# Kernel optimization log

Hardware: AMD Instinct MI355X
Metric: run time of the kernel (lower is better)

The kernel has to match this reference:

```python
import jax, jax.numpy as jnp
import numpy as np

G = 8192          # graphs in batch
A = 5             # num_agents (nodes per graph)
N = G * A         # total nodes
IN_CH = 29
HID = 64
HEADS = 8
D = HID * HEADS   # 512, node/graph feature dim
NOPT = 4
ADIM = 3


def _lin(key, fan_in, fan_out):
    return jax.random.normal(key, (fan_in, fan_out), jnp.float32) / np.sqrt(fan_in)


def setup_inputs() -> dict:
    key = jax.random.key(0)
    ks = jax.random.split(key, 40)
    # --- graph structure: G fully-connected 5-node graphs + self loops ---
    pairs = np.array([(i, j) for i in range(A) for j in range(A) if i != j])  # [20,2]
    base = (np.arange(G)[:, None] * A)
    src = (base + pairs[None, :, 0]).reshape(-1)
    dst = (base + pairs[None, :, 1]).reshape(-1)
    # GATConv adds self loops (fill_value=0.0 for edge_attr)
    loop = np.arange(N)
    edge_src = jnp.asarray(np.concatenate([src, loop]), jnp.int32)
    edge_dst = jnp.asarray(np.concatenate([dst, loop]), jnp.int32)
    e_real = jax.random.uniform(ks[0], (src.shape[0], 1), jnp.float32)
    edge_attr = jnp.concatenate([e_real, jnp.zeros((N, 1), jnp.float32)], axis=0)
    batch_map = jnp.asarray(np.repeat(np.arange(G), A), jnp.int32)
    x = jax.random.normal(ks[1], (N, IN_CH), jnp.float32)
    sc = 1.0 / np.sqrt(HID)
    inp = dict(
        x=x, edge_attr=edge_attr, edge_src=edge_src, edge_dst=edge_dst, batch_map=batch_map,
        # conv1
        W1=_lin(ks[2], IN_CH, D), as1=jax.random.normal(ks[3], (HEADS, HID)) * sc,
        ad1=jax.random.normal(ks[4], (HEADS, HID)) * sc, We1=_lin(ks[5], 1, D),
        ae1=jax.random.normal(ks[6], (HEADS, HID)) * sc, b1=jnp.zeros((D,), jnp.float32),
        # conv2
        W2=_lin(ks[7], D, D), as2=jax.random.normal(ks[8], (HEADS, HID)) * sc,
        ad2=jax.random.normal(ks[9], (HEADS, HID)) * sc, We2=_lin(ks[10], 1, D),
        ae2=jax.random.normal(ks[11], (HEADS, HID)) * sc, b2=jnp.zeros((D,), jnp.float32),
        # policy-over-options head
        pw1=_lin(ks[12], D, 2 * HID), pb1=jnp.zeros((2 * HID,)), pw2=_lin(ks[13], 2 * HID, NOPT), pb2=jnp.zeros((NOPT,)),
        # q-options head
        qw1=_lin(ks[14], D, 2 * HID), qb1=jnp.zeros((2 * HID,)), qw2=_lin(ks[15], 2 * HID, NOPT), qb2=jnp.zeros((NOPT,)),
        # intra-option actor head (option 0), input dim = node + graph feature = 2*D
        aw1=_lin(ks[16], 2 * D, 2 * HID), ab1=jnp.zeros((2 * HID,)), aw2=_lin(ks[17], 2 * HID, 2 * ADIM), ab2=jnp.zeros((2 * ADIM,)),
        # termination head (option 0)
        tw1=_lin(ks[18], D, HID), tb1=jnp.zeros((HID,)), tw2=_lin(ks[19], HID, 1), tb2=jnp.zeros((1,)),
        action_limits=jnp.array([1.0, 1.0, 3.14159], jnp.float32),
    )
    return inp


def _gat(x, src, dst, eattr, W, a_s, a_d, We, a_e, b):
    n = x.shape[0]
    h = (x @ W).reshape(n, HEADS, HID)                      # [N,H,C]
    e = (eattr @ We).reshape(-1, HEADS, HID)                # [E,H,C]
    lg = ((h * a_s).sum(-1)[src] + (h * a_d).sum(-1)[dst]
          + (e * a_e).sum(-1))                              # [E,H]
    lg = jnp.where(lg > 0, lg, 0.2 * lg)                    # leaky_relu(0.2)
    m = jax.ops.segment_max(lg, dst, num_segments=n)
    p = jnp.exp(lg - m[dst])
    denom = jax.ops.segment_sum(p, dst, num_segments=n)[dst] + 1e-16
    alpha = p / denom                                       # scatter-softmax over dst
    out = jax.ops.segment_sum(alpha[:, :, None] * h[src], dst, num_segments=n)
    return out.reshape(n, HEADS * HID) + b


def reference(x, edge_attr, edge_src, edge_dst, batch_map,
              W1, as1, ad1, We1, ae1, b1,
              W2, as2, ad2, We2, ae2, b2,
              pw1, pb1, pw2, pb2, qw1, qb1, qw2, qb2,
              aw1, ab1, aw2, ab2, tw1, tb1, tw2, tb2, action_limits):
    h = jax.nn.relu(_gat(x, edge_src, edge_dst, edge_attr, W1, as1, ad1, We1, ae1, b1))
    h = jax.nn.relu(_gat(h, edge_src, edge_dst, edge_attr, W2, as2, ad2, We2, ae2, b2))
    # global_mean_pool
    cnt = jax.ops.segment_sum(jnp.ones((h.shape[0],), h.dtype), batch_map, num_segments=G)
    g = jax.ops.segment_sum(h, batch_map, num_segments=G) / cnt[:, None]   # [G,D]
    pi = jax.nn.relu(g @ pw1 + pb1) @ pw2 + pb2                            # [G,NOPT]
    q = jax.nn.relu(g @ qw1 + qb1) @ qw2 + qb2                             # [G,NOPT]
    term = jax.nn.sigmoid(jax.nn.relu(g @ tw1 + tb1) @ tw2 + tb2)          # [G,1]
    # per-graph first num_agents nodes == all nodes here (5 per graph)
    agent = h.reshape(G, A, D)
    comb = jnp.concatenate([agent, jnp.broadcast_to(g[:, None, :], (G, A, D))], axis=-1)
    ho = jax.nn.relu(comb @ aw1 + ab1) @ aw2 + ab2                          # [G,A,6]
    mean_raw, log_std_raw = jnp.split(ho, 2, axis=-1)
    mean = jnp.tanh(mean_raw) * action_limits                               # [G,A,3]
    std = 0.05 + jax.nn.sigmoid(log_std_raw) * 0.45 + 1e-6
    return jnp.concatenate([pi, q, term, mean.reshape(G, -1), std.reshape(G, -1)], axis=1)
```

## Files before the change

kernel.cpp:

```cpp
#include <hip/hip_runtime.h>
#include <hip/hip_bf16.h>
#include <math.h>

#define GG 8192
#define AA 5
#define NN (GG * AA)
#define DD 512

typedef unsigned short ushort_t;
typedef unsigned int uint_t;

__device__ inline float bf2f(ushort_t u) {
  union { uint_t i; float f; } c; c.i = ((uint_t)u) << 16; return c.f;
}
__device__ inline ushort_t f2bf(float f) {
  union { float f; uint_t i; } c; c.f = f;
  uint_t r = c.i + 0x7fffu + ((c.i >> 16) & 1u);
  return (ushort_t)(r >> 16);
}

using frag8 = __attribute__((ext_vector_type(8))) short;
using f32x4 = __attribute__((ext_vector_type(4))) float;

typedef __attribute__((address_space(3))) void lds_void;
typedef __attribute__((address_space(1))) const void gbl_void;
#define GLL(g, l) __builtin_amdgcn_global_load_lds((gbl_void*)(g), (lds_void*)(l), 16, 0, 0)

__device__ inline int xcd_swz(int bid, int nwg) {
  return (bid & 7) * (nwg >> 3) + (bid >> 3);
}

__global__ __launch_bounds__(256) void k_prep(
    const float* __restrict__ x, const float* __restrict__ W1,
    const float* __restrict__ W2, const float* __restrict__ pw1,
    const float* __restrict__ qw1, const float* __restrict__ tw1,
    const float* __restrict__ aw1, const float* __restrict__ pb1,
    const float* __restrict__ qb1, const float* __restrict__ tb1,
    const float* __restrict__ ab1, const float* __restrict__ We1,
    const float* __restrict__ ae1, const float* __restrict__ We2,
    const float* __restrict__ ae2, const float* __restrict__ as1,
    const float* __restrict__ ad1, const float* __restrict__ as2,
    const float* __restrict__ ad2, const float* __restrict__ pw2,
    const float* __restrict__ pb2, const float* __restrict__ qw2,
    const float* __restrict__ qb2, const float* __restrict__ tw2,
    const float* __restrict__ tb2, const float* __restrict__ aw2,
    const float* __restrict__ ab2, ushort_t* __restrict__ xpad32,
    ushort_t* __restrict__ W1T32, ushort_t* __restrict__ W2T,
    ushort_t* __restrict__ WcatT, ushort_t* __restrict__ aw1topT,
    ushort_t* __restrict__ wsc1T, ushort_t* __restrict__ wsc2T,
    float* __restrict__ bcat, float* __restrict__ sce,
    float* __restrict__ woutT, float* __restrict__ bout) {
  int b = blockIdx.x;
  int t = threadIdx.x;
  if (b < 1024) {
    int i = b * 256 + t;
    int n = i >> 9, k = i & 511;
    W2T[(size_t)n * 512 + k] = f2bf(W2[(size_t)k * 512 + n]);
    float v;
    if (n < 128)      v = pw1[(size_t)k * 128 + n];
    else if (n < 256) v = qw1[(size_t)k * 128 + (n - 128)];
    else if (n < 320) v = tw1[(size_t)k * 64 + (n - 256)];
    else if (n < 448) v = aw1[(size_t)(512 + k) * 128 + (n - 320)];
    else              v = 0.f;
    WcatT[(size_t)n * 512 + k] = f2bf(v);
    if (n < 128) aw1topT[(size_t)n * 512 + k] = f2bf(aw1[(size_t)k * 128 + n]);
    if (k == 0) {
      float bv;
      if (n < 128)      bv = pb1[n];
      else if (n < 256) bv = qb1[n - 128];
      else if (n < 320) bv = tb1[n - 256];
      else if (n < 448) bv = ab1[n - 320];
      else              bv = 0.f;
      bcat[n] = bv;
    }
    if (i < 512 * 32) {
      int nn = i >> 5, kk = i & 31;
      W1T32[i] = (kk < 29) ? f2bf(W1[(size_t)kk * 512 + nn]) : (ushort_t)0;
    }
    if (i < 16384) {
      int k2 = i & 511, srow = i >> 9;
      int nh2 = srow >> 4, s = srow & 15;
      float val = 0.f;
      if (s < 8) {
        int head = nh2 * 4 + (s >> 1);
        const float* av = ((s & 1) ? ad2 : as2) + head * 64;
        const float* wr = W2 + (size_t)k2 * 512 + head * 64;
        for (int c = 0; c < 64; ++c) val = fmaf(wr[c], av[c], val);
      }
      wsc2T[i] = f2bf(val);
    }
    if (i < 1024) {
      int k1 = i & 31, srow = i >> 5;
      int nh1 = srow >> 4, s = srow & 15;
      float val = 0.f;
      if (s < 8 && k1 < 29) {
        int head = nh1 * 4 + (s >> 1);
        const float* av = ((s & 1) ? ad1 : as1) + head * 64;
        const float* wr = W1 + (size_t)k1 * 512 + head * 64;
        for (int c = 0; c < 64; ++c) val = fmaf(wr[c], av[c], val);
      }
      wsc1T[i] = f2bf(val);
    }
    if (i < 16) {
      int h = i & 7;
      const float* Wp = (i < 8) ? We1 : We2;
      const float* ap = (i < 8) ? ae1 : ae2;
      float c = 0.f;
      for (int k2 = 0; k2 < 64; ++k2) c = fmaf(Wp[h * 64 + k2], ap[h * 64 + k2], c);
      sce[i] = c;
    }
    if (i < 5120) {
      int j = i / 40, o = i % 40;
      float wv;
      if (o < 4)       wv = pw2[j * 4 + o];
      else if (o < 8)  wv = qw2[j * 4 + (o - 4)];
      else if (o == 8) wv = (j < 64) ? tw2[j] : 0.f;
      else if (o < 24) wv = aw2[j * 6 + (o - 9) % 3];
      else if (o < 39) wv = aw2[j * 6 + 3 + (o - 24) % 3];
      else             wv = 0.f;
      woutT[i] = wv;
      if (j == 0) {
        float bv;
        if (o < 4)       bv = pb2[o];
        else if (o < 8)  bv = qb2[o - 4];
        else if (o == 8) bv = tb2[0];
        else if (o < 24) bv = ab2[(o - 9) % 3];
        else if (o < 39) bv = ab2[3 + (o - 24) % 3];
        else             bv = 0.f;
        bout[o] = bv;
      }
    }
  } else {
    int i = (b - 1024) * 256 + t;
    int n = i >> 5, k = i & 31;
    xpad32[i] = (k < 29) ? f2bf(x[(size_t)n * 29 + k]) : (ushort_t)0;
  }
}

template <int KDIM, bool POOL>
__global__ __launch_bounds__(512) void k_fused(
    const ushort_t* __restrict__ A, const ushort_t* __restrict__ BT,
    const ushort_t* __restrict__ WS, const float* __restrict__ eattr,
    const float* __restrict__ sce, const float* __restrict__ bvec,
    ushort_t* __restrict__ hout, ushort_t* __restrict__ gmean) {
  __shared__ __align__(16) char smem[54016];
  const int t = threadIdx.x;
  const int lane = t & 63;
  const int w = t >> 6;
  const int l15 = lane & 15;
  const int ko2 = ((((lane >> 4) ^ (lane & 3) ^ ((lane >> 2) & 3)) & 3) * 16);
  int lid = xcd_swz(blockIdx.x, gridDim.x);
  const int mb = lid >> 1, nh = lid & 1;
  const int m0 = mb * 80;
  const int g0 = mb * 16;
  const int n0 = nh * 256;
  const ushort_t* WSn = WS + (size_t)nh * 16 * KDIM;
  constexpr int nt = KDIM / 32;
  f32x4 acc[5][2] = {};
  f32x4 asc[5] = {};
#define FSTAGE(bi, kk0)                                                        \
  {                                                                            \
    char* bb_ = smem + (bi) * 16384;                                           \
    char* aa_ = smem + 32768 + (bi) * 5120;                                    \
    char* sb_ = smem + 43008 + (bi) * 1024;                                    \
    _Pragma("unroll")                                                          \
    for (int r_ = 0; r_ < 2; ++r_) {                                           \
      int c_ = t + r_ * 512; int row_ = c_ >> 2;                               \
      int sw_ = ((((c_ & 3) ^ (row_ & 3) ^ ((row_ >> 2) & 3)) & 3)) * 8;       \
      GLL(BT + (size_t)(n0 + row_) * KDIM + (kk0) + sw_, bb_ + c_ * 16);       \
    }                                                                          \
    if (t < 320) {                                                             \
      int c_ = t; int row_ = c_ >> 2;                                          \
      int sw_ = ((((c_ & 3) ^ (row_ & 3) ^ ((row_ >> 2) & 3)) & 3)) * 8;       \
      GLL(A + (size_t)(m0 + row_) * KDIM + (kk0) + sw_, aa_ + c_ * 16);        \
    } else if (t < 384) {                                                      \
      int c_ = t - 320; int row_ = c_ >> 2;                                    \
      int sw_ = ((((c_ & 3) ^ (row_ & 3) ^ ((row_ >> 2) & 3)) & 3)) * 8;       \
      GLL(WSn + (size_t)row_ * KDIM + (kk0) + sw_, sb_ + c_ * 16);             \
    }                                                                          \
  }
  FSTAGE(0, 0);
  for (int ts = 0; ts < nt; ++ts) {
    int cur = ts & 1;
    if (ts + 1 < nt) {
      FSTAGE(cur ^ 1, (ts + 1) * 32);
      if (w < 6) { asm volatile("s_waitcnt vmcnt(3)" ::: "memory"); }
      else       { asm volatile("s_waitcnt vmcnt(2)" ::: "memory"); }
    } else {
      asm volatile("s_waitcnt vmcnt(0)" ::: "memory");
    }
    __builtin_amdgcn_s_barrier();
    __builtin_amdgcn_sched_barrier(0);
    const char* bb = smem + cur * 16384;
    const char* aa = smem + 32768 + cur * 5120;
    const char* sb = smem + 43008 + cur * 1024;
    frag8 af[5], bfr[2];
#pragma unroll
    for (int mt = 0; mt < 5; ++mt)
      af[mt] = *(const frag8*)(aa + (mt * 16 + l15) * 64 + ko2);
#pragma unroll
    for (int n = 0; n < 2; ++n)
      bfr[n] = *(const frag8*)(bb + ((2 * w + n) * 16 + l15) * 64 + ko2);
    __builtin_amdgcn_s_setprio(1);
#pragma unroll
    for (int mt = 0; mt < 5; ++mt)
#pragma unroll
      for (int n = 0; n < 2; ++n)
        acc[mt][n] = __builtin_amdgcn_mfma_f32_16x16x32_bf16(af[mt], bfr[n], acc[mt][n], 0, 0, 0);
    if (w == 7) {
      frag8 sfr = *(const frag8*)(sb + l15 * 64 + ko2);
#pragma unroll
      for (int mt = 0; mt < 5; ++mt)
        asc[mt] = __builtin_amdgcn_mfma_f32_16x16x32_bf16(af[mt], sfr, asc[mt], 0, 0, 0);
    }
    __builtin_amdgcn_s_setprio(0);
    __builtin_amdgcn_sched_barrier(0);
    __builtin_amdgcn_s_barrier();
  }
#undef FSTAGE
  ushort_t* hb = (ushort_t*)smem;
  {
    int q4 = (lane >> 4) * 4;
#pragma unroll
    for (int mt = 0; mt < 5; ++mt)
#pragma unroll
      for (int n = 0; n < 2; ++n) {
        int col = (2 * w + n) * 16 + l15;
        int hd = col >> 6, cc = col & 63;
#pragma unroll
        for (int r = 0; r < 4; ++r)
          hb[(mt * 16 + q4 + r) * 280 + hd * 70 + cc] = f2bf(acc[mt][n][r]);
      }
    if (w == 7 && l15 < 8) {
      float* dst = (float*)(smem + ((lane & 1) ? 46336 : 45056));
      int hd = l15 >> 1;
#pragma unroll
      for (int mt = 0; mt < 5; ++mt)
#pragma unroll
        for (int r = 0; r < 4; ++r)
          dst[(mt * 16 + q4 + r) * 4 + hd] = asc[mt][r];
    }
  }
  __syncthreads();
  float* sss = (float*)(smem + 45056);
  float* ssd = (float*)(smem + 46336);
  float* sal = (float*)(smem + 47616);
  if (t < 320) {
    int gi = t / 20, jh = t % 20;
    int j = jh >> 2, hd = jh & 3;
    int g = g0 + gi;
    float sdj = ssd[(gi * 5 + j) * 4 + hd];
    float ce = sce[nh * 4 + hd];
    float lg[5], mx = -1e30f;
#pragma unroll
    for (int i = 0; i < 5; ++i) {
      float l = sss[(gi * 5 + i) * 4 + hd] + sdj;
      if (i != j) l = fmaf(eattr[(size_t)g * 20 + i * 4 + (j > i ? j - 1 : j)], ce, l);
      l = l > 0.f ? l : 0.2f * l;
      lg[i] = l; mx = fmaxf(mx, l);
    }
    float s = 0.f;
#pragma unroll
    for (int i = 0; i < 5; ++i) { lg[i] = __expf(lg[i] - mx); s += lg[i]; }
    float inv = 1.f / (s + 1e-16f);
#pragma unroll
    for (int i = 0; i < 5; ++i) sal[((gi * 5 + j) * 5 + i) * 4 + hd] = lg[i] * inv;
  }
  __syncthreads();
  for (int u = t; u < 1024; u += 512) {
    int gi = u >> 6, cq = u & 63;
    int hd = cq >> 4, cc4 = (cq & 15) * 4;
    float hv[5][4];
#pragma unroll
    for (int i = 0; i < 5; ++i) {
      const char* pb = (const char*)hb + (size_t)((gi * 5 + i) * 280 + hd * 70 + cc4) * 2;
      uint_t u0 = *(const uint_t*)pb;
      uint_t u1 = *(const uint_t*)(pb + 4);
      hv[i][0] = bf2f((ushort_t)(u0 & 0xffff));
      hv[i][1] = bf2f((ushort_t)(u0 >> 16));
      hv[i][2] = bf2f((ushort_t)(u1 & 0xffff));
      hv[i][3] = bf2f((ushort_t)(u1 >> 16));
    }
    float4 bb4 = *(const float4*)&bvec[n0 + cq * 4];
    float gs0 = 0.f, gs1 = 0.f, gs2 = 0.f, gs3 = 0.f;
#pragma unroll
    for (int j = 0; j < 5; ++j) {
      float o0 = bb4.x, o1 = bb4.y, o2 = bb4.z, o3 = bb4.w;
#pragma unroll
      for (int i = 0; i < 5; ++i) {
        float a = sal[((gi * 5 + j) * 5 + i) * 4 + hd];
        o0 = fmaf(a, hv[i][0], o0); o1 = fmaf(a, hv[i][1], o1);
        o2 = fmaf(a, hv[i][2], o2); o3 = fmaf(a, hv[i][3], o3);
      }
      o0 = fmaxf(o0, 0.f); o1 = fmaxf(o1, 0.f);
      o2 = fmaxf(o2, 0.f); o3 = fmaxf(o3, 0.f);
      uint2 wv_;
      wv_.x = (uint_t)f2bf(o0) | ((uint_t)f2bf(o1) << 16);
      wv_.y = (uint_t)f2bf(o2) | ((uint_t)f2bf(o3) << 16);
      *(uint2*)(hout + ((size_t)(g0 + gi) * 5 + j) * 512 + n0 + cq * 4) = wv_;
      if (POOL) { gs0 += o0; gs1 += o1; gs2 += o2; gs3 += o3; }
    }
    if (POOL) {
      uint2 wv_;
      wv_.x = (uint_t)f2bf(gs0 * 0.2f) | ((uint_t)f2bf(gs1 * 0.2f) << 16);
      wv_.y = (uint_t)f2bf(gs2 * 0.2f) | ((uint_t)f2bf(gs3 * 0.2f) << 16);
      *(uint2*)(gmean + (size_t)(g0 + gi) * 512 + n0 + cq * 4) = wv_;
    }
  }
}

template <int EPI>
__device__ __forceinline__ void gemm_body(
    const ushort_t* __restrict__ A, const ushort_t* __restrict__ BT,
    const float* __restrict__ bias, void* __restrict__ Cv,
    int M, int N, int K, int m0, int n0, char* lds) {
  int t = threadIdx.x;
  int lane = t & 63;
  int wv = t >> 6;
  int wr = (wv >> 1) * 64, wc = (wv & 1) * 64;
  f32x4 acc[4][4] = {};
  int ch0 = t, ch1 = t + 256;
  int row0 = ch0 >> 2, row1 = ch1 >> 2;
  int sw0 = (((ch0 & 3) ^ (row0 & 3) ^ ((row0 >> 2) & 3)) & 3) * 8;
  int sw1 = (((ch1 & 3) ^ (row1 & 3) ^ ((row1 >> 2) & 3)) & 3) * 8;
  int ko2 = ((((lane >> 4) ^ (lane & 3) ^ ((lane >> 2) & 3)) & 3) * 16);
  const int nt = K >> 5;
#define STAGE(bi, kk0)                                                         \
  {                                                                            \
    char* ab = lds + (bi) * 16384;                                             \
    GLL(A + (size_t)(m0 + row0) * K + (kk0) + sw0, ab + ch0 * 16);             \
    GLL(A + (size_t)(m0 + row1) * K + (kk0) + sw1, ab + ch1 * 16);             \
    GLL(BT + (size_t)(n0 + row0) * K + (kk0) + sw0, ab + 8192 + ch0 * 16);     \
    GLL(BT + (size_t)(n0 + row1) * K + (kk0) + sw1, ab + 8192 + ch1 * 16);     \
  }
  STAGE(0, 0);
  if (nt > 1) STAGE(1, 32);
  for (int ts = 0; ts < nt; ++ts) {
    int bi = ts % 3;
    if (ts + 2 < nt) {
      STAGE((ts + 2) % 3, (ts + 2) * 32);
      asm volatile("s_waitcnt vmcnt(8)" ::: "memory");
    } else if (ts + 1 < nt) {
      asm volatile("s_waitcnt vmcnt(4)" ::: "memory");
    } else {
      asm volatile("s_waitcnt vmcnt(0)" ::: "memory");
    }
    __builtin_amdgcn_s_barrier();
    __builtin_amdgcn_sched_barrier(0);
    const char* ab = lds + bi * 16384;
    frag8 af[4], bfr[4];
#pragma unroll
    for (int m = 0; m < 4; ++m)
      af[m] = *(const frag8*)(ab + (wr + m * 16 + (lane & 15)) * 64 + ko2);
#pragma unroll
    for (int n = 0; n < 4; ++n)
      bfr[n] = *(const frag8*)(ab + 8192 + (wc + n * 16 + (lane & 15)) * 64 + ko2);
#pragma unroll
    for (int m = 0; m < 4; ++m)
#pragma unroll
      for (int n = 0; n < 4; ++n)
        acc[m][n] = __builtin_amdgcn_mfma_f32_16x16x32_bf16(af[m], bfr[n], acc[m][n], 0, 0, 0);
    __builtin_amdgcn_sched_barrier(0);
    __builtin_amdgcn_s_barrier();
  }
#undef STAGE
  int r4 = (lane >> 4) * 4;
  int cl = lane & 15;
#pragma unroll
  for (int m = 0; m < 4; ++m) {
#pragma unroll
    for (int n = 0; n < 4; ++n) {
      int col = n0 + wc + n * 16 + cl;
      float bb = (EPI == 2) ? bias[col] : 0.f;
#pragma unroll
      for (int r = 0; r < 4; ++r) {
        int row = m0 + wr + m * 16 + r4 + r;
        float v = acc[m][n][r] + bb;
        if (EPI == 2 && col < 320) v = fmaxf(v, 0.f);
        ((float*)Cv)[(size_t)row * N + col] = v;
      }
    }
  }
}

__global__ __launch_bounds__(256) void k_hgemm(
    const ushort_t* __restrict__ h2, const ushort_t* __restrict__ aw1topT,
    float* __restrict__ ahid, const ushort_t* __restrict__ gmean,
    const ushort_t* __restrict__ WcatT, const float* __restrict__ bcat,
    float* __restrict__ hcat) {
  __shared__ char lds[49152];
  int bid = blockIdx.x;
  if (bid < 320) {
    int lid = xcd_swz(bid, 320);
    gemm_body<1>(h2, aw1topT, nullptr, ahid, NN, 128, DD, lid * 128, 0, lds);
  } else {
    int lid = xcd_swz(bid - 320, 256);
    gemm_body<2>(gmean, WcatT, bcat, hcat, GG, DD, DD, (lid >> 2) * 128, (lid & 3) * 128, lds);
  }
}

__global__ __launch_bounds__(256) void k_heads(
    const float* __restrict__ hcat, const float* __restrict__ ahid,
    const float* __restrict__ woutT, const float* __restrict__ bout,
    const float* __restrict__ alim, float* __restrict__ out) {
  int g0 = blockIdx.x * 4;
  int t = threadIdx.x;
  __shared__ float sbuf[4224];
  for (int i = t; i < 4224; i += 256) {
    int gi = i / 1056, r = i - gi * 1056;
    const float* grow = hcat + (size_t)(g0 + gi) * 512;
    float v = 0.f;
    if (r < 128)                  v = grow[r];
    else if (r >= 132 && r < 260) v = grow[128 + r - 132];
    else if (r >= 264 && r < 328) v = grow[256 + r - 264];
    else if (r >= 396) {
      int q = r - 396; int a = q / 132; int j = q - a * 132;
      if (j < 128)
        v = fmaxf(ahid[((size_t)(g0 + gi) * 5 + a) * 128 + j] + grow[320 + j], 0.f);
    }
    sbuf[i] = v;
  }
  __syncthreads();
  int gi = t >> 6, o = t & 63;
  int oc = o < 39 ? o : 39;
  int seg;
  if (oc < 4)       seg = 0;
  else if (oc < 8)  seg = 132;
  else if (oc == 8) seg = 264;
  else {
    int idx = (oc < 24) ? oc - 9 : oc - 24;
    seg = 396 + (idx / 3) * 132;
  }
  const float* ip = &sbuf[gi * 1056 + seg];
  float a0 = 0.f, a1 = 0.f, a2 = 0.f, a3 = 0.f;
#pragma unroll
  for (int j = 0; j < 128; j += 4) {
    a0 = fmaf(ip[j + 0], woutT[(j + 0) * 40 + oc], a0);
    a1 = fmaf(ip[j + 1], woutT[(j + 1) * 40 + oc], a1);
    a2 = fmaf(ip[j + 2], woutT[(j + 2) * 40 + oc], a2);
    a3 = fmaf(ip[j + 3], woutT[(j + 3) * 40 + oc], a3);
  }
  float res = (a0 + a1) + (a2 + a3) + bout[oc];
  if (o < 39) {
    if (o == 8)       res = 1.f / (1.f + __expf(-res));
    else if (o >= 24) res = 0.05f + 0.45f / (1.f + __expf(-res)) + 1e-6f;
    else if (o >= 9)  res = tanhf(res) * alim[(o - 9) % 3];
    out[(size_t)(g0 + gi) * 39 + o] = res;
  }
}

extern "C" void kernel_launch(void* const* d_in, const int* in_sizes, int n_in,
                              void* d_out, int out_size, void* d_ws, size_t ws_size,
                              hipStream_t stream) {
  const float* x     = (const float*)d_in[0];
  const float* eattr = (const float*)d_in[1];
  const float* W1  = (const float*)d_in[5];
  const float* as1 = (const float*)d_in[6];
  const float* ad1 = (const float*)d_in[7];
  const float* We1 = (const float*)d_in[8];
  const float* ae1 = (const float*)d_in[9];
  const float* b1  = (const float*)d_in[10];
  const float* W2  = (const float*)d_in[11];
  const float* as2 = (const float*)d_in[12];
  const float* ad2 = (const float*)d_in[13];
  const float* We2 = (const float*)d_in[14];
  const float* ae2 = (const float*)d_in[15];
  const float* b2  = (const float*)d_in[16];
  const float* pw1 = (const float*)d_in[17];
  const float* pb1 = (const float*)d_in[18];
  const float* pw2 = (const float*)d_in[19];
  const float* pb2 = (const float*)d_in[20];
  const float* qw1 = (const float*)d_in[21];
  const float* qb1 = (const float*)d_in[22];
  const float* qw2 = (const float*)d_in[23];
  const float* qb2 = (const float*)d_in[24];
  const float* aw1 = (const float*)d_in[25];
  const float* ab1 = (const float*)d_in[26];
  const float* aw2 = (const float*)d_in[27];
  const float* ab2 = (const float*)d_in[28];
  const float* tw1 = (const float*)d_in[29];
  const float* tb1 = (const float*)d_in[30];
  const float* tw2 = (const float*)d_in[31];
  const float* tb2 = (const float*)d_in[32];
  const float* alim = (const float*)d_in[33];

  const size_t BIGE = (size_t)NN * DD;
  char* p = (char*)d_ws;
  ushort_t* h1     = (ushort_t*)p; p += BIGE * 2;
  ushort_t* h2     = (ushort_t*)p; p += BIGE * 2;
  ushort_t* gmean  = (ushort_t*)p; p += (size_t)GG * DD * 2;
  ushort_t* xpad32 = (ushort_t*)p; p += (size_t)NN * 32 * 2;
  ushort_t* W1T32  = (ushort_t*)p; p += (size_t)512 * 32 * 2;
  ushort_t* W2T    = (ushort_t*)p; p += (size_t)512 * 512 * 2;
  ushort_t* WcatT  = (ushort_t*)p; p += (size_t)512 * 512 * 2;
  ushort_t* aw1topT = (ushort_t*)p; p += (size_t)128 * 512 * 2;
  ushort_t* wsc1T  = (ushort_t*)p; p += (size_t)2 * 16 * 32 * 2;
  ushort_t* wsc2T  = (ushort_t*)p; p += (size_t)2 * 16 * 512 * 2;
  float* bcat  = (float*)p; p += 512 * 4;
  float* sce   = (float*)p; p += 16 * 4;
  float* woutT = (float*)p; p += 5120 * 4;
  float* bout  = (float*)p; p += 40 * 4;
  float* ahid  = (float*)p; p += (size_t)NN * 128 * 4;
  float* hcat  = (float*)p;

  k_prep<<<1024 + 5120, 256, 0, stream>>>(
      x, W1, W2, pw1, qw1, tw1, aw1, pb1, qb1, tb1, ab1,
      We1, ae1, We2, ae2, as1, ad1, as2, ad2,
      pw2, pb2, qw2, qb2, tw2, tb2, aw2, ab2,
      xpad32, W1T32, W2T, WcatT, aw1topT, wsc1T, wsc2T,
      bcat, sce, woutT, bout);
  k_fused<32, false><<<(NN / 80) * 2, 512, 0, stream>>>(
      xpad32, W1T32, wsc1T, eattr, sce, b1, h1, nullptr);
  k_fused<512, true><<<(NN / 80) * 2, 512, 0, stream>>>(
      h1, W2T, wsc2T, eattr, sce + 8, b2, h2, gmean);
  k_hgemm<<<320 + 256, 256, 0, stream>>>(h2, aw1topT, ahid, gmean, WcatT, bcat, hcat);
  k_heads<<<GG / 4, 256, 0, stream>>>(hcat, ahid, woutT, bout, alim, (float*)d_out);
}
```

Baseline: 114.2 us.

## Split fused GAT kernels into four 128-column slices per row block

```diff
diff --git a/kernel.cpp b/kernel.cpp
--- a/kernel.cpp
+++ b/kernel.cpp
@@ -77,24 +77,24 @@
       int nn = i >> 5, kk = i & 31;
       W1T32[i] = (kk < 29) ? f2bf(W1[(size_t)kk * 512 + nn]) : (ushort_t)0;
     }
-    if (i < 16384) {
+    if (i < 32768) {
       int k2 = i & 511, srow = i >> 9;
-      int nh2 = srow >> 4, s = srow & 15;
+      int q = srow >> 4, s = srow & 15;
       float val = 0.f;
-      if (s < 8) {
-        int head = nh2 * 4 + (s >> 1);
+      if (s < 4) {
+        int head = q * 2 + (s >> 1);
         const float* av = ((s & 1) ? ad2 : as2) + head * 64;
         const float* wr = W2 + (size_t)k2 * 512 + head * 64;
         for (int c = 0; c < 64; ++c) val = fmaf(wr[c], av[c], val);
       }
       wsc2T[i] = f2bf(val);
     }
-    if (i < 1024) {
+    if (i < 2048) {
       int k1 = i & 31, srow = i >> 5;
-      int nh1 = srow >> 4, s = srow & 15;
+      int q = srow >> 4, s = srow & 15;
       float val = 0.f;
-      if (s < 8 && k1 < 29) {
-        int head = nh1 * 4 + (s >> 1);
+      if (s < 4 && k1 < 29) {
+        int head = q * 2 + (s >> 1);
         const float* av = ((s & 1) ? ad1 : as1) + head * 64;
         const float* wr = W1 + (size_t)k1 * 512 + head * 64;
         for (int c = 0; c < 64; ++c) val = fmaf(wr[c], av[c], val);
@@ -143,29 +143,28 @@
     const ushort_t* __restrict__ WS, const float* __restrict__ eattr,
     const float* __restrict__ sce, const float* __restrict__ bvec,
     ushort_t* __restrict__ hout, ushort_t* __restrict__ gmean) {
-  __shared__ __align__(16) char smem[54016];
+  __shared__ __align__(16) char smem[28672];
   const int t = threadIdx.x;
   const int lane = t & 63;
   const int w = t >> 6;
   const int l15 = lane & 15;
   const int ko2 = ((((lane >> 4) ^ (lane & 3) ^ ((lane >> 2) & 3)) & 3) * 16);
   int lid = xcd_swz(blockIdx.x, gridDim.x);
-  const int mb = lid >> 1, nh = lid & 1;
+  const int mb = lid >> 2, nh = lid & 3;
   const int m0 = mb * 80;
   const int g0 = mb * 16;
-  const int n0 = nh * 256;
+  const int n0 = nh * 128;
   const ushort_t* WSn = WS + (size_t)nh * 16 * KDIM;
   constexpr int nt = KDIM / 32;
-  f32x4 acc[5][2] = {};
+  f32x4 acc[5] = {};
   f32x4 asc[5] = {};
 #define FSTAGE(bi, kk0)                                                        \
   {                                                                            \
-    char* bb_ = smem + (bi) * 16384;                                           \
-    char* aa_ = smem + 32768 + (bi) * 5120;                                    \
-    char* sb_ = smem + 43008 + (bi) * 1024;                                    \
-    _Pragma("unroll")                                                          \
-    for (int r_ = 0; r_ < 2; ++r_) {                                           \
-      int c_ = t + r_ * 512; int row_ = c_ >> 2;                               \
+    char* bb_ = smem + (bi) * 8192;                                            \
+    char* aa_ = smem + 16384 + (bi) * 5120;                                    \
+    char* sb_ = smem + 26624 + (bi) * 1024;                                    \
+    {                                                                          \
+      int c_ = t; int row_ = c_ >> 2;                                          \
       int sw_ = ((((c_ & 3) ^ (row_ & 3) ^ ((row_ >> 2) & 3)) & 3)) * 8;       \
       GLL(BT + (size_t)(n0 + row_) * KDIM + (kk0) + sw_, bb_ + c_ * 16);       \
     }                                                                          \
@@ -184,29 +183,25 @@
     int cur = ts & 1;
     if (ts + 1 < nt) {
       FSTAGE(cur ^ 1, (ts + 1) * 32);
-      if (w < 6) { asm volatile("s_waitcnt vmcnt(3)" ::: "memory"); }
-      else       { asm volatile("s_waitcnt vmcnt(2)" ::: "memory"); }
+      if (w < 6) { asm volatile("s_waitcnt vmcnt(2)" ::: "memory"); }
+      else       { asm volatile("s_waitcnt vmcnt(1)" ::: "memory"); }
     } else {
       asm volatile("s_waitcnt vmcnt(0)" ::: "memory");
     }
     __builtin_amdgcn_s_barrier();
     __builtin_amdgcn_sched_barrier(0);
-    const char* bb = smem + cur * 16384;
-    const char* aa = smem + 32768 + cur * 5120;
-    const char* sb = smem + 43008 + cur * 1024;
-    frag8 af[5], bfr[2];
+    const char* bb = smem + cur * 8192;
+    const char* aa = smem + 16384 + cur * 5120;
+    const char* sb = smem + 26624 + cur * 1024;
+    frag8 af[5];
 #pragma unroll
     for (int mt = 0; mt < 5; ++mt)
       af[mt] = *(const frag8*)(aa + (mt * 16 + l15) * 64 + ko2);
-#pragma unroll
-    for (int n = 0; n < 2; ++n)
-      bfr[n] = *(const frag8*)(bb + ((2 * w + n) * 16 + l15) * 64 + ko2);
+    frag8 bfr = *(const frag8*)(bb + (w * 16 + l15) * 64 + ko2);
     __builtin_amdgcn_s_setprio(1);
 #pragma unroll
     for (int mt = 0; mt < 5; ++mt)
-#pragma unroll
-      for (int n = 0; n < 2; ++n)
-        acc[mt][n] = __builtin_amdgcn_mfma_f32_16x16x32_bf16(af[mt], bfr[n], acc[mt][n], 0, 0, 0);
+      acc[mt] = __builtin_amdgcn_mfma_f32_16x16x32_bf16(af[mt], bfr, acc[mt], 0, 0, 0);
     if (w == 7) {
       frag8 sfr = *(const frag8*)(sb + l15 * 64 + ko2);
 #pragma unroll
@@ -221,40 +216,37 @@
   ushort_t* hb = (ushort_t*)smem;
   {
     int q4 = (lane >> 4) * 4;
+    int col = w * 16 + l15;
+    int hd = col >> 6, cc = col & 63;
 #pragma unroll
     for (int mt = 0; mt < 5; ++mt)
 #pragma unroll
-      for (int n = 0; n < 2; ++n) {
-        int col = (2 * w + n) * 16 + l15;
-        int hd = col >> 6, cc = col & 63;
+      for (int r = 0; r < 4; ++r)
+        hb[(mt * 16 + q4 + r) * 140 + hd * 70 + cc] = f2bf(acc[mt][r]);
+    if (w == 7 && l15 < 4) {
+      float* dst = (float*)(smem + ((l15 & 1) ? 23168 : 22528));
+      int hl = l15 >> 1;
+#pragma unroll
+      for (int mt = 0; mt < 5; ++mt)
 #pragma unroll
         for (int r = 0; r < 4; ++r)
-          hb[(mt * 16 + q4 + r) * 280 + hd * 70 + cc] = f2bf(acc[mt][n][r]);
-      }
-    if (w == 7 && l15 < 8) {
-      float* dst = (float*)(smem + ((lane & 1) ? 46336 : 45056));
-      int hd = l15 >> 1;
-#pragma unroll
-      for (int mt = 0; mt < 5; ++mt)
-#pragma unroll
-        for (int r = 0; r < 4; ++r)
-          dst[(mt * 16 + q4 + r) * 4 + hd] = asc[mt][r];
+          dst[(mt * 16 + q4 + r) * 2 + hl] = asc[mt][r];
     }
   }
   __syncthreads();
-  float* sss = (float*)(smem + 45056);
-  float* ssd = (float*)(smem + 46336);
-  float* sal = (float*)(smem + 47616);
-  if (t < 320) {
-    int gi = t / 20, jh = t % 20;
-    int j = jh >> 2, hd = jh & 3;
+  float* sss = (float*)(smem + 22528);
+  float* ssd = (float*)(smem + 23168);
+  float* sal = (float*)(smem + 23808);
+  if (t < 160) {
+    int gi = t / 10, jh = t % 10;
+    int j = jh >> 1, hd = jh & 1;
     int g = g0 + gi;
-    float sdj = ssd[(gi * 5 + j) * 4 + hd];
-    float ce = sce[nh * 4 + hd];
+    float sdj = ssd[(gi * 5 + j) * 2 + hd];
+    float ce = sce[nh * 2 + hd];
     float lg[5], mx = -1e30f;
 #pragma unroll
     for (int i = 0; i < 5; ++i) {
-      float l = sss[(gi * 5 + i) * 4 + hd] + sdj;
+      float l = sss[(gi * 5 + i) * 2 + hd] + sdj;
       if (i != j) l = fmaf(eattr[(size_t)g * 20 + i * 4 + (j > i ? j - 1 : j)], ce, l);
       l = l > 0.f ? l : 0.2f * l;
       lg[i] = l; mx = fmaxf(mx, l);
@@ -264,16 +256,16 @@
     for (int i = 0; i < 5; ++i) { lg[i] = __expf(lg[i] - mx); s += lg[i]; }
     float inv = 1.f / (s + 1e-16f);
 #pragma unroll
-    for (int i = 0; i < 5; ++i) sal[((gi * 5 + j) * 5 + i) * 4 + hd] = lg[i] * inv;
+    for (int i = 0; i < 5; ++i) sal[((gi * 5 + j) * 5 + i) * 2 + hd] = lg[i] * inv;
   }
   __syncthreads();
-  for (int u = t; u < 1024; u += 512) {
-    int gi = u >> 6, cq = u & 63;
+  {
+    int gi = t >> 5, cq = t & 31;
     int hd = cq >> 4, cc4 = (cq & 15) * 4;
     float hv[5][4];
 #pragma unroll
     for (int i = 0; i < 5; ++i) {
-      const char* pb = (const char*)hb + (size_t)((gi * 5 + i) * 280 + hd * 70 + cc4) * 2;
+      const char* pb = (const char*)hb + (size_t)((gi * 5 + i) * 140 + hd * 70 + cc4) * 2;
       uint_t u0 = *(const uint_t*)pb;
       uint_t u1 = *(const uint_t*)(pb + 4);
       hv[i][0] = bf2f((ushort_t)(u0 & 0xffff));
@@ -288,7 +280,7 @@
       float o0 = bb4.x, o1 = bb4.y, o2 = bb4.z, o3 = bb4.w;
 #pragma unroll
       for (int i = 0; i < 5; ++i) {
-        float a = sal[((gi * 5 + j) * 5 + i) * 4 + hd];
+        float a = sal[((gi * 5 + j) * 5 + i) * 2 + hd];
         o0 = fmaf(a, hv[i][0], o0); o1 = fmaf(a, hv[i][1], o1);
         o2 = fmaf(a, hv[i][2], o2); o3 = fmaf(a, hv[i][3], o3);
       }
@@ -494,8 +486,8 @@
   ushort_t* W2T    = (ushort_t*)p; p += (size_t)512 * 512 * 2;
   ushort_t* WcatT  = (ushort_t*)p; p += (size_t)512 * 512 * 2;
   ushort_t* aw1topT = (ushort_t*)p; p += (size_t)128 * 512 * 2;
-  ushort_t* wsc1T  = (ushort_t*)p; p += (size_t)2 * 16 * 32 * 2;
-  ushort_t* wsc2T  = (ushort_t*)p; p += (size_t)2 * 16 * 512 * 2;
+  ushort_t* wsc1T  = (ushort_t*)p; p += (size_t)4 * 16 * 32 * 2;
+  ushort_t* wsc2T  = (ushort_t*)p; p += (size_t)4 * 16 * 512 * 2;
   float* bcat  = (float*)p; p += 512 * 4;
   float* sce   = (float*)p; p += 16 * 4;
   float* woutT = (float*)p; p += 5120 * 4;
@@ -509,9 +501,9 @@
       pw2, pb2, qw2, qb2, tw2, tb2, aw2, ab2,
       xpad32, W1T32, W2T, WcatT, aw1topT, wsc1T, wsc2T,
       bcat, sce, woutT, bout);
-  k_fused<32, false><<<(NN / 80) * 2, 512, 0, stream>>>(
+  k_fused<32, false><<<(NN / 80) * 4, 512, 0, stream>>>(
       xpad32, W1T32, wsc1T, eattr, sce, b1, h1, nullptr);
-  k_fused<512, true><<<(NN / 80) * 2, 512, 0, stream>>>(
+  k_fused<512, true><<<(NN / 80) * 4, 512, 0, stream>>>(
       h1, W2T, wsc2T, eattr, sce + 8, b2, h2, gmean);
   k_hgemm<<<320 + 256, 256, 0, stream>>>(h2, aw1topT, ahid, gmean, WcatT, bcat, hcat);
   k_heads<<<GG / 4, 256, 0, stream>>>(hcat, ahid, woutT, bout, alim, (float*)d_out);
```

New measurement: 115.6 us. Within noise of the previous version (+1.2%).

## Keep GAT accumulators in fp32 LDS halves and overlap softmax with staging

Applied to the files above, without the earlier changes.

```diff
diff --git a/kernel.cpp b/kernel.cpp
--- a/kernel.cpp
+++ b/kernel.cpp
@@ -158,6 +158,9 @@
   constexpr int nt = KDIM / 32;
   f32x4 acc[5][2] = {};
   f32x4 asc[5] = {};
+  float* sss = (float*)(smem + 45056);
+  float* ssd = (float*)(smem + 46336);
+  float* sal = (float*)(smem + 47616);
 #define FSTAGE(bi, kk0)                                                        \
   {                                                                            \
     char* bb_ = smem + (bi) * 16384;                                           \
@@ -215,73 +218,85 @@
     }
     __builtin_amdgcn_s_setprio(0);
     __builtin_amdgcn_sched_barrier(0);
-    __builtin_amdgcn_s_barrier();
-  }
-#undef FSTAGE
-  ushort_t* hb = (ushort_t*)smem;
-  {
-    int q4 = (lane >> 4) * 4;
-#pragma unroll
-    for (int mt = 0; mt < 5; ++mt)
-#pragma unroll
-      for (int n = 0; n < 2; ++n) {
-        int col = (2 * w + n) * 16 + l15;
-        int hd = col >> 6, cc = col & 63;
-#pragma unroll
-        for (int r = 0; r < 4; ++r)
-          hb[(mt * 16 + q4 + r) * 280 + hd * 70 + cc] = f2bf(acc[mt][n][r]);
-      }
-    if (w == 7 && l15 < 8) {
-      float* dst = (float*)(smem + ((lane & 1) ? 46336 : 45056));
+    if (ts == nt - 1 && w == 7 && l15 < 8) {
+      float* dst = (lane & 1) ? ssd : sss;
       int hd = l15 >> 1;
+      int q4 = (lane >> 4) * 4;
 #pragma unroll
       for (int mt = 0; mt < 5; ++mt)
 #pragma unroll
         for (int r = 0; r < 4; ++r)
           dst[(mt * 16 + q4 + r) * 4 + hd] = asc[mt][r];
     }
+    __builtin_amdgcn_s_barrier();
+  }
+#undef FSTAGE
+  float* hbf = (float*)smem;
+  {
+    if (w < 4) {
+      int q4 = (lane >> 4) * 4;
+#pragma unroll
+      for (int mt = 0; mt < 5; ++mt)
+#pragma unroll
+        for (int n = 0; n < 2; ++n) {
+          int lc = w * 32 + n * 16 + l15;
+#pragma unroll
+          for (int r = 0; r < 4; ++r)
+            hbf[(mt * 16 + q4 + r) * 132 + lc] = acc[mt][n][r];
+        }
+    } else if (t - 256 < 160) {
+      int u = t - 256;
+      int gi = u / 10, jh = u % 10;
+      int j = jh >> 1, hd0 = jh & 1;
+#pragma unroll
+      for (int hh = 0; hh < 2; ++hh) {
+        int hd = hd0 + hh * 2;
+        int g = g0 + gi;
+        float sdj = ssd[(gi * 5 + j) * 4 + hd];
+        float ce = sce[nh * 4 + hd];
+        float lg[5], mx = -1e30f;
+#pragma unroll
+        for (int i = 0; i < 5; ++i) {
+          float l = sss[(gi * 5 + i) * 4 + hd] + sdj;
+          if (i != j) l = fmaf(eattr[(size_t)g * 20 + i * 4 + (j > i ? j - 1 : j)], ce, l);
+          l = l > 0.f ? l : 0.2f * l;
+          lg[i] = l; mx = fmaxf(mx, l);
+        }
+        float s = 0.f;
+#pragma unroll
+        for (int i = 0; i < 5; ++i) { lg[i] = __expf(lg[i] - mx); s += lg[i]; }
+        float inv = 1.f / (s + 1e-16f);
+#pragma unroll
+        for (int i = 0; i < 5; ++i) sal[((gi * 5 + j) * 5 + i) * 4 + hd] = lg[i] * inv;
+      }
+    }
   }
   __syncthreads();
-  float* sss = (float*)(smem + 45056);
-  float* ssd = (float*)(smem + 46336);
-  float* sal = (float*)(smem + 47616);
-  if (t < 320) {
-    int gi = t / 20, jh = t % 20;
-    int j = jh >> 2, hd = jh & 3;
-    int g = g0 + gi;
-    float sdj = ssd[(gi * 5 + j) * 4 + hd];
-    float ce = sce[nh * 4 + hd];
-    float lg[5], mx = -1e30f;
-#pragma unroll
-    for (int i = 0; i < 5; ++i) {
-      float l = sss[(gi * 5 + i) * 4 + hd] + sdj;
-      if (i != j) l = fmaf(eattr[(size_t)g * 20 + i * 4 + (j > i ? j - 1 : j)], ce, l);
-      l = l > 0.f ? l : 0.2f * l;
-      lg[i] = l; mx = fmaxf(mx, l);
-    }
-    float s = 0.f;
-#pragma unroll
-    for (int i = 0; i < 5; ++i) { lg[i] = __expf(lg[i] - mx); s += lg[i]; }
-    float inv = 1.f / (s + 1e-16f);
-#pragma unroll
-    for (int i = 0; i < 5; ++i) sal[((gi * 5 + j) * 5 + i) * 4 + hd] = lg[i] * inv;
-  }
-  __syncthreads();
-  for (int u = t; u < 1024; u += 512) {
-    int gi = u >> 6, cq = u & 63;
-    int hd = cq >> 4, cc4 = (cq & 15) * 4;
+#pragma unroll
+  for (int half = 0; half < 2; ++half) {
+    if (half == 1) {
+      if (w >= 4) {
+        int q4 = (lane >> 4) * 4;
+#pragma unroll
+        for (int mt = 0; mt < 5; ++mt)
+#pragma unroll
+          for (int n = 0; n < 2; ++n) {
+            int lc = (w - 4) * 32 + n * 16 + l15;
+#pragma unroll
+            for (int r = 0; r < 4; ++r)
+              hbf[(mt * 16 + q4 + r) * 132 + lc] = acc[mt][n][r];
+          }
+      }
+      __syncthreads();
+    }
+    int gi = t >> 5, cq = t & 31;
+    int hd = half * 2 + (cq >> 4);
+    int colg = n0 + half * 128 + cq * 4;
     float hv[5][4];
 #pragma unroll
-    for (int i = 0; i < 5; ++i) {
-      const char* pb = (const char*)hb + (size_t)((gi * 5 + i) * 280 + hd * 70 + cc4) * 2;
-      uint_t u0 = *(const uint_t*)pb;
-      uint_t u1 = *(const uint_t*)(pb + 4);
-      hv[i][0] = bf2f((ushort_t)(u0 & 0xffff));
-      hv[i][1] = bf2f((ushort_t)(u0 >> 16));
-      hv[i][2] = bf2f((ushort_t)(u1 & 0xffff));
-      hv[i][3] = bf2f((ushort_t)(u1 >> 16));
-    }
-    float4 bb4 = *(const float4*)&bvec[n0 + cq * 4];
+    for (int i = 0; i < 5; ++i)
+      *(float4*)hv[i] = *(const float4*)&hbf[(gi * 5 + i) * 132 + cq * 4];
+    float4 bb4 = *(const float4*)&bvec[colg];
     float gs0 = 0.f, gs1 = 0.f, gs2 = 0.f, gs3 = 0.f;
 #pragma unroll
     for (int j = 0; j < 5; ++j) {
@@ -297,15 +312,16 @@
       uint2 wv_;
       wv_.x = (uint_t)f2bf(o0) | ((uint_t)f2bf(o1) << 16);
       wv_.y = (uint_t)f2bf(o2) | ((uint_t)f2bf(o3) << 16);
-      *(uint2*)(hout + ((size_t)(g0 + gi) * 5 + j) * 512 + n0 + cq * 4) = wv_;
+      *(uint2*)(hout + ((size_t)(g0 + gi) * 5 + j) * 512 + colg) = wv_;
       if (POOL) { gs0 += o0; gs1 += o1; gs2 += o2; gs3 += o3; }
     }
     if (POOL) {
       uint2 wv_;
       wv_.x = (uint_t)f2bf(gs0 * 0.2f) | ((uint_t)f2bf(gs1 * 0.2f) << 16);
       wv_.y = (uint_t)f2bf(gs2 * 0.2f) | ((uint_t)f2bf(gs3 * 0.2f) << 16);
-      *(uint2*)(gmean + (size_t)(g0 + gi) * 512 + n0 + cq * 4) = wv_;
-    }
+      *(uint2*)(gmean + (size_t)(g0 + gi) * 512 + colg) = wv_;
+    }
+    if (half == 0) __syncthreads();
   }
 }
 
```

Result: no change. 114.0 us (-0.1%).
